# Optimization experiments

Measured on AMD Instinct MI355X. Metric: run time of the kernel, lower is better.

Reference implementation:

```python
import jax, jax.numpy as jnp
import numpy as np

B, S, D, H = 32, 2048, 512, 512

def setup_inputs() -> dict:
    key = jax.random.key(0)
    kx, kq, kk, kv = jax.random.split(key, 4)
    scale = 1.0 / np.sqrt(D)
    x = jax.random.normal(kx, (B, S, D), dtype=jnp.float32)
    Wq = jax.random.normal(kq, (D, H), dtype=jnp.float32) * scale
    Wk = jax.random.normal(kk, (D, H), dtype=jnp.float32) * scale
    Wv = jax.random.normal(kv, (D, H), dtype=jnp.float32) * scale
    return {"x": x, "Wq": Wq, "Wk": Wk, "Wv": Wv}

def reference(x, Wq, Wk, Wv):
    # Linear projections (bias=False)
    q = jnp.einsum('bsd,dh->bsh', x, Wq)
    k = jnp.einsum('bsd,dh->bsh', x, Wk)
    v = jnp.einsum('bsd,dh->bsh', x, Wv)
    # Pairwise KL(p_i || q_j) with p = softmax(q_i), q = softmax(k_j):
    #   KL = sum_h p_i log p_i  -  sum_h p_i log q_j
    # The first term is a per-row negative entropy; the second is a GEMM,
    # avoiding the original O(S^2) Python double loop.
    logp = jax.nn.log_softmax(q, axis=-1)          # [B,S,H]
    p = jnp.exp(logp)
    logq = jax.nn.log_softmax(k, axis=-1)          # [B,S,H]
    neg_ent = jnp.sum(p * logp, axis=-1)           # [B,S]
    cross = jnp.einsum('bih,bjh->bij', p, logq)    # [B,S,S]
    kl_divs = neg_ent[:, :, None] - cross          # [B,S,S]
    attn_weights = jax.nn.softmax(-kl_divs, axis=-1)
    attn_output = jnp.einsum('bij,bjh->bih', attn_weights, v)
    return attn_output
```

## Files before the change

kernel.cpp:

```cpp
#include <hip/hip_runtime.h>
#include <hip/hip_bf16.h>

typedef __bf16 bf16x8 __attribute__((ext_vector_type(8)));
typedef float  f32x4  __attribute__((ext_vector_type(4)));

#define NB 32
#define NS 2048
#define ND 512
#define NH 512
#define NROWS (NB*NS)
#define L2E 1.44269504f

__device__ __forceinline__ void gload16(const void* g, void* l) {
  __builtin_amdgcn_global_load_lds((const __attribute__((address_space(1))) void*)g,
                                   (__attribute__((address_space(3))) void*)l, 16, 0, 0);
}

__global__ void prep_w(const float* __restrict__ Wq, const float* __restrict__ Wk,
                       const float* __restrict__ Wv, __bf16* __restrict__ wT) {
  int i = blockIdx.x * blockDim.x + threadIdx.x;
  const int total = 3 * ND * NH;
  for (; i < total; i += gridDim.x * blockDim.x) {
    int m = i / (ND * NH);
    int rem = i - m * (ND * NH);
    int h = rem >> 9;
    int d = rem & 511;
    const float* W = (m == 0) ? Wq : ((m == 1) ? Wk : Wv);
    wT[i] = (__bf16)W[(size_t)d * NH + h];
  }
}

#define K1_XOFF 0
#define K1_WOFF 65536
#define K1_REDM 131072
#define K1_REDS 132096
#define K1_LDS  133120

__global__ __launch_bounds__(512, 2)
void proj_kernel(const float* __restrict__ x, const __bf16* __restrict__ wT,
                 __bf16* __restrict__ p_out, __bf16* __restrict__ k_out,
                 float* __restrict__ L_out, __bf16* __restrict__ vt_out)
{
  __shared__ __align__(16) char smem[K1_LDS];
  char* xb = smem + K1_XOFF;
  char* wb = smem + K1_WOFF;
  float* redm = (float*)(smem + K1_REDM);
  float* reds = (float*)(smem + K1_REDS);

  const int tid = threadIdx.x;
  const int lane = tid & 63, l15 = lane & 15, g = lane >> 4;
  const int w = tid >> 6, rt = w & 1, cs = w >> 1;
  const int r0 = blockIdx.x * 64;
  const int b = r0 >> 11, s0 = r0 & (NS - 1);

  {
    int row = tid >> 3, sc = tid & 7;
    const float* xr = x + (size_t)(r0 + row) * ND;
    #pragma unroll
    for (int u = 0; u < 8; ++u) {
      int s = u * 8 + sc;
      float4 v0 = *(const float4*)(xr + s * 8);
      float4 v1 = *(const float4*)(xr + s * 8 + 4);
      bf16x8 cv;
      cv[0]=(__bf16)v0.x; cv[1]=(__bf16)v0.y; cv[2]=(__bf16)v0.z; cv[3]=(__bf16)v0.w;
      cv[4]=(__bf16)v1.x; cv[5]=(__bf16)v1.y; cv[6]=(__bf16)v1.z; cv[7]=(__bf16)v1.w;
      *(bf16x8*)(xb + row * 1024 + ((s ^ (row & 7)) * 16)) = cv;
    }
  }
  {
    #pragma unroll
    for (int u = 0; u < 4; ++u) {
      int sid = u * 512 + tid, h = sid >> 2, gg = sid & 3;
      gload16(wT + (size_t)h * ND + ((gg ^ ((h >> 1) & 3)) * 8), wb + sid * 16);
    }
  }
  __syncthreads();

  for (int m = 0; m < 3; ++m) {
    f32x4 acc[2][8];
    #pragma unroll
    for (int i2 = 0; i2 < 2; ++i2)
      #pragma unroll
      for (int ht = 0; ht < 8; ++ht) acc[i2][ht] = (f32x4){0.f,0.f,0.f,0.f};

    for (int step = 0; step < 16; ++step) {
      int gs = m * 16 + step;
      char* wcur = wb + (gs & 1) * 32768;
      if (gs + 1 < 48) {
        int gn = gs + 1, mn = gn >> 4, sn = gn & 15;
        const __bf16* wsrc = wT + (size_t)mn * (ND * NH) + sn * 32;
        char* wdst = wb + (gn & 1) * 32768;
        #pragma unroll
        for (int u = 0; u < 4; ++u) {
          int sid = u * 512 + tid, h = sid >> 2, gg = sid & 3;
          gload16(wsrc + (size_t)h * ND + ((gg ^ ((h >> 1) & 3)) * 8), wdst + sid * 16);
        }
      }
      bf16x8 a0, a1;
      {
        int ar = rt * 32 + l15;
        a0 = *(const bf16x8*)(xb + ar * 1024 + (((step * 4 + g) ^ (ar & 7)) * 16));
        ar += 16;
        a1 = *(const bf16x8*)(xb + ar * 1024 + (((step * 4 + g) ^ (ar & 7)) * 16));
      }
      #pragma unroll
      for (int ht = 0; ht < 8; ++ht) {
        int h = cs * 128 + ht * 16 + l15;
        bf16x8 bb = *(const bf16x8*)(wcur + h * 64 + ((g ^ ((h >> 1) & 3)) * 16));
        acc[0][ht] = __builtin_amdgcn_mfma_f32_16x16x32_bf16(a0, bb, acc[0][ht], 0, 0, 0);
        acc[1][ht] = __builtin_amdgcn_mfma_f32_16x16x32_bf16(a1, bb, acc[1][ht], 0, 0, 0);
      }
      __syncthreads();
    }

    if (m == 2) {
      #pragma unroll
      for (int i2 = 0; i2 < 2; ++i2) {
        int sgg = (s0 >> 3) + rt * 4 + i2 * 2 + (g >> 1);
        size_t basep = ((size_t)(b * 256 + sgg)) * 512;
        #pragma unroll
        for (int ht = 0; ht < 8; ++ht) {
          int h = cs * 128 + ht * 16 + l15;
          union { __bf16 h4[4]; ushort4 u4; } cv;
          #pragma unroll
          for (int r = 0; r < 4; ++r) cv.h4[r] = (__bf16)acc[i2][ht][r];
          *(ushort4*)(vt_out + (basep + h) * 8 + (g & 1) * 4) = cv.u4;
        }
      }
    } else {
      float mrow[2][4], tsum[2][4];
      #pragma unroll
      for (int i2 = 0; i2 < 2; ++i2)
        #pragma unroll
        for (int r = 0; r < 4; ++r) {
          float v = acc[i2][0][r];
          #pragma unroll
          for (int ht = 1; ht < 8; ++ht) v = fmaxf(v, acc[i2][ht][r]);
          v = fmaxf(v, __shfl_xor(v, 1)); v = fmaxf(v, __shfl_xor(v, 2));
          v = fmaxf(v, __shfl_xor(v, 4)); v = fmaxf(v, __shfl_xor(v, 8));
          if (l15 == 0) redm[cs * 64 + rt * 32 + i2 * 16 + g * 4 + r] = v;
        }
      __syncthreads();
      #pragma unroll
      for (int i2 = 0; i2 < 2; ++i2)
        #pragma unroll
        for (int r = 0; r < 4; ++r) {
          int row = rt * 32 + i2 * 16 + g * 4 + r;
          mrow[i2][r] = fmaxf(fmaxf(redm[row], redm[64 + row]),
                              fmaxf(redm[128 + row], redm[192 + row]));
        }
      #pragma unroll
      for (int i2 = 0; i2 < 2; ++i2)
        #pragma unroll
        for (int r = 0; r < 4; ++r) {
          float s = 0.f;
          #pragma unroll
          for (int ht = 0; ht < 8; ++ht) s += exp2f((acc[i2][ht][r] - mrow[i2][r]) * L2E);
          s += __shfl_xor(s, 1); s += __shfl_xor(s, 2);
          s += __shfl_xor(s, 4); s += __shfl_xor(s, 8);
          if (l15 == 0) reds[cs * 64 + rt * 32 + i2 * 16 + g * 4 + r] = s;
        }
      __syncthreads();
      #pragma unroll
      for (int i2 = 0; i2 < 2; ++i2)
        #pragma unroll
        for (int r = 0; r < 4; ++r) {
          int row = rt * 32 + i2 * 16 + g * 4 + r;
          tsum[i2][r] = reds[row] + reds[64 + row] + reds[128 + row] + reds[192 + row];
        }
      __bf16* dst = (m == 0) ? p_out : k_out;
      if (m == 0) {
        #pragma unroll
        for (int i2 = 0; i2 < 2; ++i2) {
          float inv[4];
          #pragma unroll
          for (int r = 0; r < 4; ++r) inv[r] = 1.f / tsum[i2][r];
          #pragma unroll
          for (int ht = 0; ht < 8; ++ht) {
            int col = cs * 128 + ht * 16 + l15;
            #pragma unroll
            for (int r = 0; r < 4; ++r) {
              int row = rt * 32 + i2 * 16 + g * 4 + r;
              dst[(size_t)(r0 + row) * NH + col] =
                  (__bf16)(exp2f((acc[i2][ht][r] - mrow[i2][r]) * L2E) * inv[r]);
            }
          }
        }
      } else {
        #pragma unroll
        for (int i2 = 0; i2 < 2; ++i2)
          #pragma unroll
          for (int ht = 0; ht < 8; ++ht) {
            int col = cs * 128 + ht * 16 + l15;
            #pragma unroll
            for (int r = 0; r < 4; ++r) {
              int row = rt * 32 + i2 * 16 + g * 4 + r;
              dst[(size_t)(r0 + row) * NH + col] = (__bf16)acc[i2][ht][r];
            }
          }
        if (cs == 0 && l15 == 0) {
          #pragma unroll
          for (int i2 = 0; i2 < 2; ++i2)
            #pragma unroll
            for (int r = 0; r < 4; ++r) {
              int row = rt * 32 + i2 * 16 + g * 4 + r;
              L_out[r0 + row] = mrow[i2][r] + __logf(tsum[i2][r]);
            }
        }
      }
      __syncthreads();
    }
  }
}

#define QOFF 0
#define KOFF 65536
#define PSTR 512
#define LOFF 131072
#define LREDOFF 139264
#define A_LDS 140288

__global__ __launch_bounds__(512, 2)
void attn_kernel(const __bf16* __restrict__ p_all, const __bf16* __restrict__ k_all,
                 const float* __restrict__ L_all, const __bf16* __restrict__ vt_all,
                 float* __restrict__ out)
{
  __shared__ __align__(16) char smem[A_LDS];
  char* Qb = smem + QOFF;
  char* Pb = smem + KOFF;
  float* Lld = (float*)(smem + LOFF);
  float* lred = (float*)(smem + LREDOFF);

  const int bid = blockIdx.x;
  const int b = ((bid >> 8) << 3) + (bid & 7);
  const int ib = (bid >> 3) & 31;
  const int i0 = ib * 64;

  const __bf16* Pg = p_all + (size_t)b * NS * NH;
  const __bf16* Kg = k_all + (size_t)b * NS * NH;
  const float*  Lg = L_all + (size_t)b * NS;
  const __bf16* Vg = vt_all + (size_t)b * (256 * 512 * 8);
  float* Og = out + ((size_t)b * NS + i0) * NH;

  const int tid = threadIdx.x;
  const int lane = tid & 63, l15 = lane & 15, g = lane >> 4;
  const int w = tid >> 6;
  const int ig = w >> 2, jg = w & 3;
  const int hs = w * 64;
  const int xr = l15 & 7;

  *(float4*)(Lld + tid * 4) = *(const float4*)(Lg + tid * 4);
  #pragma unroll
  for (int u = 0; u < 8; ++u) {
    int sid = u * 512 + tid, row = sid >> 6, s = sid & 63;
    int sp = (s & 56) | ((s ^ row) & 7);
    gload16(Pg + (size_t)(i0 + row) * NH + sp * 8, Qb + sid * 16);
  }

  f32x4 o_[4][4];
  #pragma unroll
  for (int it = 0; it < 4; ++it)
    #pragma unroll
    for (int ht = 0; ht < 4; ++ht) o_[it][ht] = (f32x4){0.f,0.f,0.f,0.f};
  float lsum[2][4] = {{0.f,0.f,0.f,0.f},{0.f,0.f,0.f,0.f}};

  #define STAGEK(J0, KK, DST) { \
    _Pragma("unroll") \
    for (int u_ = 0; u_ < 4; ++u_) { \
      int sid_ = u_ * 512 + tid, jj_ = sid_ >> 3, ss_ = sid_ & 7; \
      gload16(Kg + (size_t)((J0) + jj_) * NH + (KK) * 64 + ((ss_ ^ (jj_ & 7)) * 8), \
              (DST) + sid_ * 16); \
    } }

  for (int outer = 0; outer < 8; ++outer) {
    const int j0 = outer * 256;
    __syncthreads();
    STAGEK(j0, 0, smem + KOFF);
    __syncthreads();

    f32x4 acc[2][4];
    #pragma unroll
    for (int it = 0; it < 2; ++it)
      #pragma unroll
      for (int jt = 0; jt < 4; ++jt) acc[it][jt] = (f32x4){0.f,0.f,0.f,0.f};

    for (int kk = 0; kk < 8; ++kk) {
      const char* rb = smem + KOFF + (kk & 1) * 32768;
      if (kk < 7) STAGEK(j0, kk + 1, smem + KOFF + ((kk + 1) & 1) * 32768);
      #pragma unroll
      for (int sub = 0; sub < 2; ++sub) {
        bf16x8 a0, a1, bf[4];
        {
          int row = ig * 32 + l15;
          int seg = kk * 8 + ((sub * 4 + g) ^ xr);
          a0 = *(const bf16x8*)(Qb + row * 1024 + seg * 16);
          a1 = *(const bf16x8*)(Qb + (row + 16) * 1024 + seg * 16);
        }
        #pragma unroll
        for (int jt = 0; jt < 4; ++jt) {
          int j = jg * 64 + jt * 16 + l15;
          bf[jt] = *(const bf16x8*)(rb + j * 128 + (((sub * 4 + g) ^ xr) * 16));
        }
        #pragma unroll
        for (int jt = 0; jt < 4; ++jt) {
          acc[0][jt] = __builtin_amdgcn_mfma_f32_16x16x32_bf16(a0, bf[jt], acc[0][jt], 0, 0, 0);
          acc[1][jt] = __builtin_amdgcn_mfma_f32_16x16x32_bf16(a1, bf[jt], acc[1][jt], 0, 0, 0);
        }
      }
      __syncthreads();
    }

    #pragma unroll
    for (int it = 0; it < 2; ++it) {
      #pragma unroll
      for (int jt = 0; jt < 4; ++jt) {
        float LB = Lld[j0 + jg * 64 + jt * 16 + l15] * L2E;
        #pragma unroll
        for (int r = 0; r < 4; ++r) {
          float pv = exp2f(acc[it][jt][r] * L2E - LB);
          lsum[it][r] += pv;
          float other = __shfl_xor(pv, 1);
          if ((l15 & 1) == 0) {
            union { __bf16 h; unsigned short u; } lo, hi;
            lo.h = (__bf16)pv; hi.h = (__bf16)other;
            unsigned int pk = (unsigned int)lo.u | ((unsigned int)hi.u << 16);
            int row = ig * 32 + it * 16 + g * 4 + r;
            int d = jg * 32 + jt * 8 + (l15 >> 1);
            int s2 = (d >> 2) ^ (row & 7);
            *(unsigned int*)(Pb + row * PSTR + s2 * 16 + (d & 3) * 4) = pk;
          }
        }
      }
    }
    __syncthreads();

    #define LOADV(DST, JKS) { \
      _Pragma("unroll") \
      for (int ht_ = 0; ht_ < 4; ++ht_) { \
        int h_ = hs + ht_ * 16 + l15; \
        int sg_ = outer * 32 + (JKS) * 4 + g; \
        (DST)[ht_] = *(const bf16x8*)(Vg + ((size_t)sg_ * 512 + h_) * 8); \
      } }
    #define PVSTEP(JKS, VF) { \
      _Pragma("unroll") \
      for (int it_ = 0; it_ < 4; ++it_) { \
        int row_ = it_ * 16 + l15; \
        int sp_ = ((JKS) * 4 + g) ^ xr; \
        bf16x8 pa_ = *(const bf16x8*)(Pb + row_ * PSTR + sp_ * 16); \
        _Pragma("unroll") \
        for (int ht_ = 0; ht_ < 4; ++ht_) \
          o_[it_][ht_] = __builtin_amdgcn_mfma_f32_16x16x32_bf16(pa_, (VF)[ht_], o_[it_][ht_], 0, 0, 0); \
      } }

    {
      bf16x8 vA[4], vB[4];
      LOADV(vA, 0);
      #pragma unroll
      for (int jks = 0; jks < 8; jks += 2) {
        LOADV(vB, jks + 1);
        PVSTEP(jks, vA);
        if (jks + 2 < 8) LOADV(vA, jks + 2);
        PVSTEP(jks + 1, vB);
      }
    }
  }

  #pragma unroll
  for (int it = 0; it < 2; ++it)
    #pragma unroll
    for (int r = 0; r < 4; ++r) {
      float v = lsum[it][r];
      v += __shfl_xor(v, 1); v += __shfl_xor(v, 2);
      v += __shfl_xor(v, 4); v += __shfl_xor(v, 8);
      if (l15 == 0) lred[jg * 64 + ig * 32 + it * 16 + g * 4 + r] = v;
    }
  __syncthreads();

  #pragma unroll
  for (int it = 0; it < 4; ++it) {
    float inv[4];
    #pragma unroll
    for (int r = 0; r < 4; ++r) {
      int row = it * 16 + g * 4 + r;
      inv[r] = 1.f / (lred[row] + lred[64 + row] + lred[128 + row] + lred[192 + row]);
    }
    #pragma unroll
    for (int ht = 0; ht < 4; ++ht)
      #pragma unroll
      for (int r = 0; r < 4; ++r) {
        int row = it * 16 + g * 4 + r;
        Og[(size_t)row * NH + hs + ht * 16 + l15] = o_[it][ht][r] * inv[r];
      }
  }
}

extern "C" void kernel_launch(void* const* d_in, const int* in_sizes, int n_in,
                              void* d_out, int out_size, void* d_ws, size_t ws_size,
                              hipStream_t stream) {
  const float* x  = (const float*)d_in[0];
  const float* Wq = (const float*)d_in[1];
  const float* Wk = (const float*)d_in[2];
  const float* Wv = (const float*)d_in[3];
  float* out = (float*)d_out;
  char* ws = (char*)d_ws;

  size_t off = 0;
  __bf16* wT   = (__bf16*)(ws + off); off += (size_t)3 * ND * NH * 2;
  __bf16* p_ws = (__bf16*)(ws + off); off += (size_t)NROWS * NH * 2;
  __bf16* k_ws = (__bf16*)(ws + off); off += (size_t)NROWS * NH * 2;
  __bf16* vt_ws= (__bf16*)(ws + off); off += (size_t)NROWS * NH * 2;
  float*  L_ws = (float*)(ws + off);  off += (size_t)NROWS * 4;

  prep_w<<<dim3(512), dim3(256), 0, stream>>>(Wq, Wk, Wv, wT);
  proj_kernel<<<dim3(1024), dim3(512), 0, stream>>>(x, wT, p_ws, k_ws, L_ws, vt_ws);
  attn_kernel<<<dim3(1024), dim3(512), 0, stream>>>(p_ws, k_ws, L_ws, vt_ws, out);
}
```

Baseline: 760.4 us.

## Pipeline K staging across outer tiles and re-tile projection warps

In the attention kernel, P gets its own LDS region instead of aliasing the K buffer. This lets the next outer tile's first K slice be prefetched during the PV phase, removing the per-outer barrier-and-load bubble. The L values are now read directly from global memory instead of being staged in LDS, and V fragments are triple-buffered in registers. The projection kernel changes its warp tiling from 2x4 (32 rows x 128 cols) to 1x8 (64 rows x 64 cols per warp), which alters register use and LDS read traffic. The cost is more LDS per block (163840 bytes for attention), which may limit occupancy.

```diff
diff --git a/kernel.cpp b/kernel.cpp
--- a/kernel.cpp
+++ b/kernel.cpp
@@ -33,8 +33,8 @@
 #define K1_XOFF 0
 #define K1_WOFF 65536
 #define K1_REDM 131072
-#define K1_REDS 132096
-#define K1_LDS  133120
+#define K1_REDS 133120
+#define K1_LDS  135168
 
 __global__ __launch_bounds__(512, 2)
 void proj_kernel(const float* __restrict__ x, const __bf16* __restrict__ wT,
@@ -49,7 +49,7 @@
 
   const int tid = threadIdx.x;
   const int lane = tid & 63, l15 = lane & 15, g = lane >> 4;
-  const int w = tid >> 6, rt = w & 1, cs = w >> 1;
+  const int cs = tid >> 6;
   const int r0 = blockIdx.x * 64;
   const int b = r0 >> 11, s0 = r0 & (NS - 1);
 
@@ -67,144 +67,143 @@
       *(bf16x8*)(xb + row * 1024 + ((s ^ (row & 7)) * 16)) = cv;
     }
   }
-  {
-    #pragma unroll
-    for (int u = 0; u < 4; ++u) {
-      int sid = u * 512 + tid, h = sid >> 2, gg = sid & 3;
-      gload16(wT + (size_t)h * ND + ((gg ^ ((h >> 1) & 3)) * 8), wb + sid * 16);
-    }
-  }
+  #define STAGEW(GS) { \
+    int mn_ = (GS) >> 4, sn_ = (GS) & 15; \
+    const __bf16* ws_ = wT + (size_t)mn_ * (ND * NH) + sn_ * 32; \
+    char* wd_ = wb + ((GS) & 1) * 32768; \
+    _Pragma("unroll") \
+    for (int u_ = 0; u_ < 4; ++u_) { \
+      int sid_ = u_ * 512 + tid, h_ = sid_ >> 2, gg_ = sid_ & 3; \
+      gload16(ws_ + (size_t)h_ * ND + ((gg_ ^ ((h_ >> 1) & 3)) * 8), wd_ + sid_ * 16); \
+    } }
+  STAGEW(0);
   __syncthreads();
 
   for (int m = 0; m < 3; ++m) {
-    f32x4 acc[2][8];
-    #pragma unroll
-    for (int i2 = 0; i2 < 2; ++i2)
-      #pragma unroll
-      for (int ht = 0; ht < 8; ++ht) acc[i2][ht] = (f32x4){0.f,0.f,0.f,0.f};
+    f32x4 acc[4][4];
+    #pragma unroll
+    for (int it = 0; it < 4; ++it)
+      #pragma unroll
+      for (int ht = 0; ht < 4; ++ht) acc[it][ht] = (f32x4){0.f,0.f,0.f,0.f};
 
     for (int step = 0; step < 16; ++step) {
       int gs = m * 16 + step;
-      char* wcur = wb + (gs & 1) * 32768;
-      if (gs + 1 < 48) {
-        int gn = gs + 1, mn = gn >> 4, sn = gn & 15;
-        const __bf16* wsrc = wT + (size_t)mn * (ND * NH) + sn * 32;
-        char* wdst = wb + (gn & 1) * 32768;
-        #pragma unroll
-        for (int u = 0; u < 4; ++u) {
-          int sid = u * 512 + tid, h = sid >> 2, gg = sid & 3;
-          gload16(wsrc + (size_t)h * ND + ((gg ^ ((h >> 1) & 3)) * 8), wdst + sid * 16);
-        }
-      }
-      bf16x8 a0, a1;
-      {
-        int ar = rt * 32 + l15;
-        a0 = *(const bf16x8*)(xb + ar * 1024 + (((step * 4 + g) ^ (ar & 7)) * 16));
-        ar += 16;
-        a1 = *(const bf16x8*)(xb + ar * 1024 + (((step * 4 + g) ^ (ar & 7)) * 16));
-      }
-      #pragma unroll
-      for (int ht = 0; ht < 8; ++ht) {
-        int h = cs * 128 + ht * 16 + l15;
-        bf16x8 bb = *(const bf16x8*)(wcur + h * 64 + ((g ^ ((h >> 1) & 3)) * 16));
-        acc[0][ht] = __builtin_amdgcn_mfma_f32_16x16x32_bf16(a0, bb, acc[0][ht], 0, 0, 0);
-        acc[1][ht] = __builtin_amdgcn_mfma_f32_16x16x32_bf16(a1, bb, acc[1][ht], 0, 0, 0);
-      }
+      const char* wcur = wb + (gs & 1) * 32768;
+      if (gs + 1 < 48) STAGEW(gs + 1);
+      bf16x8 a[4], bq[4];
+      #pragma unroll
+      for (int it = 0; it < 4; ++it) {
+        int row = it * 16 + l15;
+        a[it] = *(const bf16x8*)(xb + row * 1024 + (((step * 4 + g) ^ (row & 7)) * 16));
+      }
+      #pragma unroll
+      for (int ht = 0; ht < 4; ++ht) {
+        int h = cs * 64 + ht * 16 + l15;
+        bq[ht] = *(const bf16x8*)(wcur + h * 64 + ((g ^ ((h >> 1) & 3)) * 16));
+      }
+      #pragma unroll
+      for (int it = 0; it < 4; ++it)
+        #pragma unroll
+        for (int ht = 0; ht < 4; ++ht)
+          acc[it][ht] = __builtin_amdgcn_mfma_f32_16x16x32_bf16(a[it], bq[ht], acc[it][ht], 0, 0, 0);
       __syncthreads();
     }
 
     if (m == 2) {
       #pragma unroll
-      for (int i2 = 0; i2 < 2; ++i2) {
-        int sgg = (s0 >> 3) + rt * 4 + i2 * 2 + (g >> 1);
+      for (int it = 0; it < 4; ++it) {
+        int sgg = (s0 >> 3) + it * 2 + (g >> 1);
         size_t basep = ((size_t)(b * 256 + sgg)) * 512;
         #pragma unroll
-        for (int ht = 0; ht < 8; ++ht) {
-          int h = cs * 128 + ht * 16 + l15;
+        for (int ht = 0; ht < 4; ++ht) {
+          int h = cs * 64 + ht * 16 + l15;
           union { __bf16 h4[4]; ushort4 u4; } cv;
           #pragma unroll
-          for (int r = 0; r < 4; ++r) cv.h4[r] = (__bf16)acc[i2][ht][r];
+          for (int r = 0; r < 4; ++r) cv.h4[r] = (__bf16)acc[it][ht][r];
           *(ushort4*)(vt_out + (basep + h) * 8 + (g & 1) * 4) = cv.u4;
         }
       }
     } else {
-      float mrow[2][4], tsum[2][4];
-      #pragma unroll
-      for (int i2 = 0; i2 < 2; ++i2)
+      #pragma unroll
+      for (int it = 0; it < 4; ++it)
         #pragma unroll
         for (int r = 0; r < 4; ++r) {
-          float v = acc[i2][0][r];
-          #pragma unroll
-          for (int ht = 1; ht < 8; ++ht) v = fmaxf(v, acc[i2][ht][r]);
+          float v = acc[it][0][r];
+          #pragma unroll
+          for (int ht = 1; ht < 4; ++ht) v = fmaxf(v, acc[it][ht][r]);
           v = fmaxf(v, __shfl_xor(v, 1)); v = fmaxf(v, __shfl_xor(v, 2));
           v = fmaxf(v, __shfl_xor(v, 4)); v = fmaxf(v, __shfl_xor(v, 8));
-          if (l15 == 0) redm[cs * 64 + rt * 32 + i2 * 16 + g * 4 + r] = v;
+          if (l15 == 0) redm[cs * 64 + it * 16 + g * 4 + r] = v;
         }
       __syncthreads();
-      #pragma unroll
-      for (int i2 = 0; i2 < 2; ++i2)
+      float mrow[4][4];
+      #pragma unroll
+      for (int it = 0; it < 4; ++it)
         #pragma unroll
         for (int r = 0; r < 4; ++r) {
-          int row = rt * 32 + i2 * 16 + g * 4 + r;
-          mrow[i2][r] = fmaxf(fmaxf(redm[row], redm[64 + row]),
-                              fmaxf(redm[128 + row], redm[192 + row]));
-        }
-      #pragma unroll
-      for (int i2 = 0; i2 < 2; ++i2)
+          int row = it * 16 + g * 4 + r;
+          float mv = redm[row];
+          #pragma unroll
+          for (int w2 = 1; w2 < 8; ++w2) mv = fmaxf(mv, redm[w2 * 64 + row]);
+          mrow[it][r] = mv;
+        }
+      #pragma unroll
+      for (int it = 0; it < 4; ++it)
         #pragma unroll
         for (int r = 0; r < 4; ++r) {
           float s = 0.f;
           #pragma unroll
-          for (int ht = 0; ht < 8; ++ht) s += exp2f((acc[i2][ht][r] - mrow[i2][r]) * L2E);
+          for (int ht = 0; ht < 4; ++ht) s += exp2f((acc[it][ht][r] - mrow[it][r]) * L2E);
           s += __shfl_xor(s, 1); s += __shfl_xor(s, 2);
           s += __shfl_xor(s, 4); s += __shfl_xor(s, 8);
-          if (l15 == 0) reds[cs * 64 + rt * 32 + i2 * 16 + g * 4 + r] = s;
+          if (l15 == 0) reds[cs * 64 + it * 16 + g * 4 + r] = s;
         }
       __syncthreads();
-      #pragma unroll
-      for (int i2 = 0; i2 < 2; ++i2)
+      float tsum[4][4];
+      #pragma unroll
+      for (int it = 0; it < 4; ++it)
         #pragma unroll
         for (int r = 0; r < 4; ++r) {
-          int row = rt * 32 + i2 * 16 + g * 4 + r;
-          tsum[i2][r] = reds[row] + reds[64 + row] + reds[128 + row] + reds[192 + row];
+          int row = it * 16 + g * 4 + r;
+          float s = reds[row];
+          #pragma unroll
+          for (int w2 = 1; w2 < 8; ++w2) s += reds[w2 * 64 + row];
+          tsum[it][r] = s;
         }
       __bf16* dst = (m == 0) ? p_out : k_out;
       if (m == 0) {
         #pragma unroll
-        for (int i2 = 0; i2 < 2; ++i2) {
-          float inv[4];
-          #pragma unroll
-          for (int r = 0; r < 4; ++r) inv[r] = 1.f / tsum[i2][r];
-          #pragma unroll
-          for (int ht = 0; ht < 8; ++ht) {
-            int col = cs * 128 + ht * 16 + l15;
+        for (int it = 0; it < 4; ++it)
+          #pragma unroll
+          for (int r = 0; r < 4; ++r) {
+            int row = it * 16 + g * 4 + r;
+            float inv = 1.f / tsum[it][r];
+            #pragma unroll
+            for (int ht = 0; ht < 4; ++ht) {
+              int col = cs * 64 + ht * 16 + l15;
+              dst[(size_t)(r0 + row) * NH + col] =
+                  (__bf16)(exp2f((acc[it][ht][r] - mrow[it][r]) * L2E) * inv);
+            }
+          }
+      } else {
+        #pragma unroll
+        for (int it = 0; it < 4; ++it)
+          #pragma unroll
+          for (int ht = 0; ht < 4; ++ht) {
+            int col = cs * 64 + ht * 16 + l15;
             #pragma unroll
             for (int r = 0; r < 4; ++r) {
-              int row = rt * 32 + i2 * 16 + g * 4 + r;
-              dst[(size_t)(r0 + row) * NH + col] =
-                  (__bf16)(exp2f((acc[i2][ht][r] - mrow[i2][r]) * L2E) * inv[r]);
-            }
-          }
-        }
-      } else {
-        #pragma unroll
-        for (int i2 = 0; i2 < 2; ++i2)
-          #pragma unroll
-          for (int ht = 0; ht < 8; ++ht) {
-            int col = cs * 128 + ht * 16 + l15;
-            #pragma unroll
-            for (int r = 0; r < 4; ++r) {
-              int row = rt * 32 + i2 * 16 + g * 4 + r;
-              dst[(size_t)(r0 + row) * NH + col] = (__bf16)acc[i2][ht][r];
+              int row = it * 16 + g * 4 + r;
+              dst[(size_t)(r0 + row) * NH + col] = (__bf16)acc[it][ht][r];
             }
           }
         if (cs == 0 && l15 == 0) {
           #pragma unroll
-          for (int i2 = 0; i2 < 2; ++i2)
+          for (int it = 0; it < 4; ++it)
             #pragma unroll
             for (int r = 0; r < 4; ++r) {
-              int row = rt * 32 + i2 * 16 + g * 4 + r;
-              L_out[r0 + row] = mrow[i2][r] + __logf(tsum[i2][r]);
+              int row = it * 16 + g * 4 + r;
+              L_out[r0 + row] = mrow[it][r] + __logf(tsum[it][r]);
             }
         }
       }
@@ -215,10 +214,9 @@
 
 #define QOFF 0
 #define KOFF 65536
+#define POFF 131072
 #define PSTR 512
-#define LOFF 131072
-#define LREDOFF 139264
-#define A_LDS 140288
+#define A_LDS 163840
 
 __global__ __launch_bounds__(512, 2)
 void attn_kernel(const __bf16* __restrict__ p_all, const __bf16* __restrict__ k_all,
@@ -227,9 +225,8 @@
 {
   __shared__ __align__(16) char smem[A_LDS];
   char* Qb = smem + QOFF;
-  char* Pb = smem + KOFF;
-  float* Lld = (float*)(smem + LOFF);
-  float* lred = (float*)(smem + LREDOFF);
+  char* Pb = smem + POFF;
+  float* lred = (float*)(smem + POFF);
 
   const int bid = blockIdx.x;
   const int b = ((bid >> 8) << 3) + (bid & 7);
@@ -249,13 +246,24 @@
   const int hs = w * 64;
   const int xr = l15 & 7;
 
-  *(float4*)(Lld + tid * 4) = *(const float4*)(Lg + tid * 4);
+  #define STAGE(SS) { \
+    int j0_ = ((SS) >> 3) * 256, kh_ = (SS) & 7; \
+    char* kd_ = smem + KOFF + ((SS) & 1) * 32768; \
+    _Pragma("unroll") \
+    for (int u_ = 0; u_ < 4; ++u_) { \
+      int sid_ = u_ * 512 + tid, jj_ = sid_ >> 3, s8_ = sid_ & 7; \
+      gload16(Kg + (size_t)(j0_ + jj_) * NH + kh_ * 64 + ((s8_ ^ (jj_ & 7)) * 8), \
+              kd_ + sid_ * 16); \
+    } }
+
   #pragma unroll
   for (int u = 0; u < 8; ++u) {
     int sid = u * 512 + tid, row = sid >> 6, s = sid & 63;
     int sp = (s & 56) | ((s ^ row) & 7);
     gload16(Pg + (size_t)(i0 + row) * NH + sp * 8, Qb + sid * 16);
   }
+  STAGE(0);
+  __syncthreads();
 
   f32x4 o_[4][4];
   #pragma unroll
@@ -264,115 +272,111 @@
     for (int ht = 0; ht < 4; ++ht) o_[it][ht] = (f32x4){0.f,0.f,0.f,0.f};
   float lsum[2][4] = {{0.f,0.f,0.f,0.f},{0.f,0.f,0.f,0.f}};
 
-  #define STAGEK(J0, KK, DST) { \
+  #define LOADV(DST, JKS) { \
     _Pragma("unroll") \
-    for (int u_ = 0; u_ < 4; ++u_) { \
-      int sid_ = u_ * 512 + tid, jj_ = sid_ >> 3, ss_ = sid_ & 7; \
-      gload16(Kg + (size_t)((J0) + jj_) * NH + (KK) * 64 + ((ss_ ^ (jj_ & 7)) * 8), \
-              (DST) + sid_ * 16); \
+    for (int ht_ = 0; ht_ < 4; ++ht_) { \
+      int h_ = hs + ht_ * 16 + l15; \
+      int sg_ = outer * 32 + (JKS) * 4 + g; \
+      (DST)[ht_] = *(const bf16x8*)(Vg + ((size_t)sg_ * 512 + h_) * 8); \
+    } }
+  #define PVSTEP(JKS, VF) { \
+    _Pragma("unroll") \
+    for (int it_ = 0; it_ < 4; ++it_) { \
+      int row_ = it_ * 16 + l15; \
+      int sp_ = ((JKS) * 4 + g) ^ xr; \
+      bf16x8 pa_ = *(const bf16x8*)(Pb + row_ * PSTR + sp_ * 16); \
+      _Pragma("unroll") \
+      for (int ht_ = 0; ht_ < 4; ++ht_) \
+        o_[it_][ht_] = __builtin_amdgcn_mfma_f32_16x16x32_bf16(pa_, (VF)[ht_], o_[it_][ht_], 0, 0, 0); \
     } }
 
   for (int outer = 0; outer < 8; ++outer) {
     const int j0 = outer * 256;
-    __syncthreads();
-    STAGEK(j0, 0, smem + KOFF);
-    __syncthreads();
-
     f32x4 acc[2][4];
     #pragma unroll
-    for (int it = 0; it < 2; ++it)
-      #pragma unroll
-      for (int jt = 0; jt < 4; ++jt) acc[it][jt] = (f32x4){0.f,0.f,0.f,0.f};
-
+    for (int i2 = 0; i2 < 2; ++i2)
+      #pragma unroll
+      for (int jt = 0; jt < 4; ++jt) acc[i2][jt] = (f32x4){0.f,0.f,0.f,0.f};
+
+    #pragma unroll
     for (int kk = 0; kk < 8; ++kk) {
-      const char* rb = smem + KOFF + (kk & 1) * 32768;
-      if (kk < 7) STAGEK(j0, kk + 1, smem + KOFF + ((kk + 1) & 1) * 32768);
-      #pragma unroll
-      for (int sub = 0; sub < 2; ++sub) {
-        bf16x8 a0, a1, bf[4];
-        {
-          int row = ig * 32 + l15;
-          int seg = kk * 8 + ((sub * 4 + g) ^ xr);
-          a0 = *(const bf16x8*)(Qb + row * 1024 + seg * 16);
-          a1 = *(const bf16x8*)(Qb + (row + 16) * 1024 + seg * 16);
-        }
+      const int ss = outer * 8 + kk;
+      if (!(kk == 0 && outer > 0) && ss < 63) STAGE(ss + 1);
+      const char* rb = smem + KOFF + (ss & 1) * 32768;
+      bf16x8 aq[2][2], bq[2][4];
+      #pragma unroll
+      for (int i2 = 0; i2 < 2; ++i2) {
+        int row = ig * 32 + i2 * 16 + l15;
+        #pragma unroll
+        for (int sub = 0; sub < 2; ++sub)
+          aq[i2][sub] = *(const bf16x8*)(Qb + row * 1024 +
+                         (((kk * 8 + sub * 4 + g) ^ (row & 7)) * 16));
+      }
+      #pragma unroll
+      for (int sub = 0; sub < 2; ++sub)
         #pragma unroll
         for (int jt = 0; jt < 4; ++jt) {
           int j = jg * 64 + jt * 16 + l15;
-          bf[jt] = *(const bf16x8*)(rb + j * 128 + (((sub * 4 + g) ^ xr) * 16));
-        }
-        #pragma unroll
-        for (int jt = 0; jt < 4; ++jt) {
-          acc[0][jt] = __builtin_amdgcn_mfma_f32_16x16x32_bf16(a0, bf[jt], acc[0][jt], 0, 0, 0);
-          acc[1][jt] = __builtin_amdgcn_mfma_f32_16x16x32_bf16(a1, bf[jt], acc[1][jt], 0, 0, 0);
-        }
-      }
+          bq[sub][jt] = *(const bf16x8*)(rb + j * 128 + (((sub * 4 + g) ^ xr) * 16));
+        }
+      #pragma unroll
+      for (int sub = 0; sub < 2; ++sub)
+        #pragma unroll
+        for (int i2 = 0; i2 < 2; ++i2)
+          #pragma unroll
+          for (int jt = 0; jt < 4; ++jt)
+            acc[i2][jt] = __builtin_amdgcn_mfma_f32_16x16x32_bf16(aq[i2][sub], bq[sub][jt], acc[i2][jt], 0, 0, 0);
       __syncthreads();
     }
 
-    #pragma unroll
-    for (int it = 0; it < 2; ++it) {
-      #pragma unroll
-      for (int jt = 0; jt < 4; ++jt) {
-        float LB = Lld[j0 + jg * 64 + jt * 16 + l15] * L2E;
-        #pragma unroll
-        for (int r = 0; r < 4; ++r) {
-          float pv = exp2f(acc[it][jt][r] * L2E - LB);
-          lsum[it][r] += pv;
-          float other = __shfl_xor(pv, 1);
-          if ((l15 & 1) == 0) {
-            union { __bf16 h; unsigned short u; } lo, hi;
-            lo.h = (__bf16)pv; hi.h = (__bf16)other;
-            unsigned int pk = (unsigned int)lo.u | ((unsigned int)hi.u << 16);
-            int row = ig * 32 + it * 16 + g * 4 + r;
-            int d = jg * 32 + jt * 8 + (l15 >> 1);
-            int s2 = (d >> 2) ^ (row & 7);
-            *(unsigned int*)(Pb + row * PSTR + s2 * 16 + (d & 3) * 4) = pk;
+    {
+      float LB[4];
+      #pragma unroll
+      for (int jt = 0; jt < 4; ++jt) LB[jt] = Lg[j0 + jg * 64 + jt * 16 + l15] * L2E;
+      #pragma unroll
+      for (int i2 = 0; i2 < 2; ++i2)
+        #pragma unroll
+        for (int jt = 0; jt < 4; ++jt)
+          #pragma unroll
+          for (int r = 0; r < 4; ++r) {
+            float pv = exp2f(acc[i2][jt][r] * L2E - LB[jt]);
+            lsum[i2][r] += pv;
+            float other = __shfl_xor(pv, 1);
+            if ((l15 & 1) == 0) {
+              union { __bf16 h; unsigned short u; } lo, hi;
+              lo.h = (__bf16)pv; hi.h = (__bf16)other;
+              unsigned int pk = (unsigned int)lo.u | ((unsigned int)hi.u << 16);
+              int row = ig * 32 + i2 * 16 + g * 4 + r;
+              int d = jg * 32 + jt * 8 + (l15 >> 1);
+              int s2 = (d >> 2) ^ (row & 7);
+              *(unsigned int*)(Pb + row * PSTR + s2 * 16 + (d & 3) * 4) = pk;
+            }
           }
-        }
-      }
-    }
+    }
+    bf16x8 vA[4], vB[4], vC[4];
+    LOADV(vA, 0); LOADV(vB, 1); LOADV(vC, 2);
     __syncthreads();
-
-    #define LOADV(DST, JKS) { \
-      _Pragma("unroll") \
-      for (int ht_ = 0; ht_ < 4; ++ht_) { \
-        int h_ = hs + ht_ * 16 + l15; \
-        int sg_ = outer * 32 + (JKS) * 4 + g; \
-        (DST)[ht_] = *(const bf16x8*)(Vg + ((size_t)sg_ * 512 + h_) * 8); \
-      } }
-    #define PVSTEP(JKS, VF) { \
-      _Pragma("unroll") \
-      for (int it_ = 0; it_ < 4; ++it_) { \
-        int row_ = it_ * 16 + l15; \
-        int sp_ = ((JKS) * 4 + g) ^ xr; \
-        bf16x8 pa_ = *(const bf16x8*)(Pb + row_ * PSTR + sp_ * 16); \
-        _Pragma("unroll") \
-        for (int ht_ = 0; ht_ < 4; ++ht_) \
-          o_[it_][ht_] = __builtin_amdgcn_mfma_f32_16x16x32_bf16(pa_, (VF)[ht_], o_[it_][ht_], 0, 0, 0); \
-      } }
-
-    {
-      bf16x8 vA[4], vB[4];
-      LOADV(vA, 0);
-      #pragma unroll
-      for (int jks = 0; jks < 8; jks += 2) {
-        LOADV(vB, jks + 1);
-        PVSTEP(jks, vA);
-        if (jks + 2 < 8) LOADV(vA, jks + 2);
-        PVSTEP(jks + 1, vB);
-      }
-    }
-  }
-
+    if (outer < 7) STAGE(outer * 8 + 9);
+
+    PVSTEP(0, vA); LOADV(vA, 3);
+    PVSTEP(1, vB); LOADV(vB, 4);
+    PVSTEP(2, vC); LOADV(vC, 5);
+    PVSTEP(3, vA); LOADV(vA, 6);
+    PVSTEP(4, vB); LOADV(vB, 7);
+    PVSTEP(5, vC);
+    PVSTEP(6, vA);
+    PVSTEP(7, vB);
+  }
+
+  __syncthreads();
   #pragma unroll
-  for (int it = 0; it < 2; ++it)
+  for (int i2 = 0; i2 < 2; ++i2)
     #pragma unroll
     for (int r = 0; r < 4; ++r) {
-      float v = lsum[it][r];
+      float v = lsum[i2][r];
       v += __shfl_xor(v, 1); v += __shfl_xor(v, 2);
       v += __shfl_xor(v, 4); v += __shfl_xor(v, 8);
-      if (l15 == 0) lred[jg * 64 + ig * 32 + it * 16 + g * 4 + r] = v;
+      if (l15 == 0) lred[jg * 64 + ig * 32 + i2 * 16 + g * 4 + r] = v;
     }
   __syncthreads();
 
```

Measured after the change: 849.6 us. 1.12x slower.

## Triple-buffer K tiles across outer iterations and overlap staging with softmax and PV

Applied to the files above, without the earlier changes.

Replaces the per-outer-iteration K double buffer with a three-slot ring that keeps two stages in flight across outer-loop boundaries. The P tile now reuses the just-consumed K slot instead of having its own region. The L values are read directly from global memory instead of a preloaded LDS copy. Full __syncthreads are replaced with explicit waitcnt plus s_barrier, and MFMA sections are wrapped in s_setprio. This is meant to hide K load latency and remove pipeline restart bubbles, at the cost of more LDS, tighter hand-managed synchronization and a risk of subtle buffer-reuse hazards.

```diff
diff --git a/kernel.cpp b/kernel.cpp
--- a/kernel.cpp
+++ b/kernel.cpp
@@ -216,9 +216,7 @@
 #define QOFF 0
 #define KOFF 65536
 #define PSTR 512
-#define LOFF 131072
-#define LREDOFF 139264
-#define A_LDS 140288
+#define A_LDS 163840
 
 __global__ __launch_bounds__(512, 2)
 void attn_kernel(const __bf16* __restrict__ p_all, const __bf16* __restrict__ k_all,
@@ -227,9 +225,7 @@
 {
   __shared__ __align__(16) char smem[A_LDS];
   char* Qb = smem + QOFF;
-  char* Pb = smem + KOFF;
-  float* Lld = (float*)(smem + LOFF);
-  float* lred = (float*)(smem + LREDOFF);
+  float* lred = (float*)(smem + KOFF);
 
   const int bid = blockIdx.x;
   const int b = ((bid >> 8) << 3) + (bid & 7);
@@ -249,13 +245,24 @@
   const int hs = w * 64;
   const int xr = l15 & 7;
 
-  *(float4*)(Lld + tid * 4) = *(const float4*)(Lg + tid * 4);
+  #define STAGE(SS) { \
+    int j0_ = ((SS) >> 3) * 256, kh_ = (SS) & 7; \
+    char* kd_ = smem + KOFF + ((SS) % 3) * 32768; \
+    _Pragma("unroll") \
+    for (int u_ = 0; u_ < 4; ++u_) { \
+      int sid_ = u_ * 512 + tid, jj_ = sid_ >> 3, s8_ = sid_ & 7; \
+      gload16(Kg + (size_t)(j0_ + jj_) * NH + kh_ * 64 + ((s8_ ^ (jj_ & 7)) * 8), \
+              kd_ + sid_ * 16); \
+    } }
+
   #pragma unroll
   for (int u = 0; u < 8; ++u) {
     int sid = u * 512 + tid, row = sid >> 6, s = sid & 63;
     int sp = (s & 56) | ((s ^ row) & 7);
     gload16(Pg + (size_t)(i0 + row) * NH + sp * 8, Qb + sid * 16);
   }
+  STAGE(0);
+  STAGE(1);
 
   f32x4 o_[4][4];
   #pragma unroll
@@ -264,115 +271,122 @@
     for (int ht = 0; ht < 4; ++ht) o_[it][ht] = (f32x4){0.f,0.f,0.f,0.f};
   float lsum[2][4] = {{0.f,0.f,0.f,0.f},{0.f,0.f,0.f,0.f}};
 
-  #define STAGEK(J0, KK, DST) { \
+  #define LOADV(DST, JKS) { \
     _Pragma("unroll") \
-    for (int u_ = 0; u_ < 4; ++u_) { \
-      int sid_ = u_ * 512 + tid, jj_ = sid_ >> 3, ss_ = sid_ & 7; \
-      gload16(Kg + (size_t)((J0) + jj_) * NH + (KK) * 64 + ((ss_ ^ (jj_ & 7)) * 8), \
-              (DST) + sid_ * 16); \
+    for (int ht_ = 0; ht_ < 4; ++ht_) { \
+      int h_ = hs + ht_ * 16 + l15; \
+      int sg_ = outer * 32 + (JKS) * 4 + g; \
+      (DST)[ht_] = *(const bf16x8*)(Vg + ((size_t)sg_ * 512 + h_) * 8); \
     } }
+  #define PVSTEP(JKS, VF) { \
+    __builtin_amdgcn_s_setprio(1); \
+    _Pragma("unroll") \
+    for (int it_ = 0; it_ < 4; ++it_) { \
+      int row_ = it_ * 16 + l15; \
+      int sp_ = ((JKS) * 4 + g) ^ xr; \
+      bf16x8 pa_ = *(const bf16x8*)(Pb + row_ * PSTR + sp_ * 16); \
+      _Pragma("unroll") \
+      for (int ht_ = 0; ht_ < 4; ++ht_) \
+        o_[it_][ht_] = __builtin_amdgcn_mfma_f32_16x16x32_bf16(pa_, (VF)[ht_], o_[it_][ht_], 0, 0, 0); \
+    } \
+    __builtin_amdgcn_s_setprio(0); }
 
   for (int outer = 0; outer < 8; ++outer) {
     const int j0 = outer * 256;
-    __syncthreads();
-    STAGEK(j0, 0, smem + KOFF);
-    __syncthreads();
-
     f32x4 acc[2][4];
     #pragma unroll
-    for (int it = 0; it < 2; ++it)
-      #pragma unroll
-      for (int jt = 0; jt < 4; ++jt) acc[it][jt] = (f32x4){0.f,0.f,0.f,0.f};
-
+    for (int i2 = 0; i2 < 2; ++i2)
+      #pragma unroll
+      for (int jt = 0; jt < 4; ++jt) acc[i2][jt] = (f32x4){0.f,0.f,0.f,0.f};
+
+    #pragma unroll
     for (int kk = 0; kk < 8; ++kk) {
-      const char* rb = smem + KOFF + (kk & 1) * 32768;
-      if (kk < 7) STAGEK(j0, kk + 1, smem + KOFF + ((kk + 1) & 1) * 32768);
+      const int ss = outer * 8 + kk;
+      asm volatile("s_waitcnt vmcnt(4)" ::: "memory");
+      __builtin_amdgcn_sched_barrier(0);
+      __builtin_amdgcn_s_barrier();
+      __builtin_amdgcn_sched_barrier(0);
+      if (ss + 2 < 64) STAGE(ss + 2);
+      const char* rb = smem + KOFF + (ss % 3) * 32768;
       #pragma unroll
       for (int sub = 0; sub < 2; ++sub) {
-        bf16x8 a0, a1, bf[4];
+        bf16x8 a0, a1, bq[4];
         {
-          int row = ig * 32 + l15;
-          int seg = kk * 8 + ((sub * 4 + g) ^ xr);
-          a0 = *(const bf16x8*)(Qb + row * 1024 + seg * 16);
-          a1 = *(const bf16x8*)(Qb + (row + 16) * 1024 + seg * 16);
+          int row0 = ig * 32 + l15;
+          int seg = kk * 8 + sub * 4 + g;
+          a0 = *(const bf16x8*)(Qb + row0 * 1024 + ((seg ^ (row0 & 7)) * 16));
+          a1 = *(const bf16x8*)(Qb + (row0 + 16) * 1024 + ((seg ^ ((row0 + 16) & 7)) * 16));
         }
         #pragma unroll
         for (int jt = 0; jt < 4; ++jt) {
           int j = jg * 64 + jt * 16 + l15;
-          bf[jt] = *(const bf16x8*)(rb + j * 128 + (((sub * 4 + g) ^ xr) * 16));
-        }
+          bq[jt] = *(const bf16x8*)(rb + j * 128 + (((sub * 4 + g) ^ xr) * 16));
+        }
+        __builtin_amdgcn_s_setprio(1);
         #pragma unroll
         for (int jt = 0; jt < 4; ++jt) {
-          acc[0][jt] = __builtin_amdgcn_mfma_f32_16x16x32_bf16(a0, bf[jt], acc[0][jt], 0, 0, 0);
-          acc[1][jt] = __builtin_amdgcn_mfma_f32_16x16x32_bf16(a1, bf[jt], acc[1][jt], 0, 0, 0);
-        }
-      }
-      __syncthreads();
-    }
-
-    #pragma unroll
-    for (int it = 0; it < 2; ++it) {
-      #pragma unroll
-      for (int jt = 0; jt < 4; ++jt) {
-        float LB = Lld[j0 + jg * 64 + jt * 16 + l15] * L2E;
-        #pragma unroll
-        for (int r = 0; r < 4; ++r) {
-          float pv = exp2f(acc[it][jt][r] * L2E - LB);
-          lsum[it][r] += pv;
-          float other = __shfl_xor(pv, 1);
-          if ((l15 & 1) == 0) {
-            union { __bf16 h; unsigned short u; } lo, hi;
-            lo.h = (__bf16)pv; hi.h = (__bf16)other;
-            unsigned int pk = (unsigned int)lo.u | ((unsigned int)hi.u << 16);
-            int row = ig * 32 + it * 16 + g * 4 + r;
-            int d = jg * 32 + jt * 8 + (l15 >> 1);
-            int s2 = (d >> 2) ^ (row & 7);
-            *(unsigned int*)(Pb + row * PSTR + s2 * 16 + (d & 3) * 4) = pk;
+          acc[0][jt] = __builtin_amdgcn_mfma_f32_16x16x32_bf16(a0, bq[jt], acc[0][jt], 0, 0, 0);
+          acc[1][jt] = __builtin_amdgcn_mfma_f32_16x16x32_bf16(a1, bq[jt], acc[1][jt], 0, 0, 0);
+        }
+        __builtin_amdgcn_s_setprio(0);
+      }
+    }
+
+    __builtin_amdgcn_sched_barrier(0);
+    __builtin_amdgcn_s_barrier();
+    __builtin_amdgcn_sched_barrier(0);
+    char* Pb = smem + KOFF + ((outer * 8 + 7) % 3) * 32768;
+
+    {
+      float LB[4];
+      #pragma unroll
+      for (int jt = 0; jt < 4; ++jt) LB[jt] = Lg[j0 + jg * 64 + jt * 16 + l15] * L2E;
+      #pragma unroll
+      for (int i2 = 0; i2 < 2; ++i2)
+        #pragma unroll
+        for (int jt = 0; jt < 4; ++jt)
+          #pragma unroll
+          for (int r = 0; r < 4; ++r) {
+            float pv = exp2f(acc[i2][jt][r] * L2E - LB[jt]);
+            lsum[i2][r] += pv;
+            float other = __shfl_xor(pv, 1);
+            if ((l15 & 1) == 0) {
+              union { __bf16 h; unsigned short u; } lo, hi;
+              lo.h = (__bf16)pv; hi.h = (__bf16)other;
+              unsigned int pk = (unsigned int)lo.u | ((unsigned int)hi.u << 16);
+              int row = ig * 32 + i2 * 16 + g * 4 + r;
+              int d = jg * 32 + jt * 8 + (l15 >> 1);
+              int s2 = (d >> 2) ^ (row & 7);
+              *(unsigned int*)(Pb + row * PSTR + s2 * 16 + (d & 3) * 4) = pk;
+            }
           }
-        }
-      }
-    }
-    __syncthreads();
-
-    #define LOADV(DST, JKS) { \
-      _Pragma("unroll") \
-      for (int ht_ = 0; ht_ < 4; ++ht_) { \
-        int h_ = hs + ht_ * 16 + l15; \
-        int sg_ = outer * 32 + (JKS) * 4 + g; \
-        (DST)[ht_] = *(const bf16x8*)(Vg + ((size_t)sg_ * 512 + h_) * 8); \
-      } }
-    #define PVSTEP(JKS, VF) { \
-      _Pragma("unroll") \
-      for (int it_ = 0; it_ < 4; ++it_) { \
-        int row_ = it_ * 16 + l15; \
-        int sp_ = ((JKS) * 4 + g) ^ xr; \
-        bf16x8 pa_ = *(const bf16x8*)(Pb + row_ * PSTR + sp_ * 16); \
-        _Pragma("unroll") \
-        for (int ht_ = 0; ht_ < 4; ++ht_) \
-          o_[it_][ht_] = __builtin_amdgcn_mfma_f32_16x16x32_bf16(pa_, (VF)[ht_], o_[it_][ht_], 0, 0, 0); \
-      } }
-
-    {
-      bf16x8 vA[4], vB[4];
-      LOADV(vA, 0);
-      #pragma unroll
-      for (int jks = 0; jks < 8; jks += 2) {
-        LOADV(vB, jks + 1);
-        PVSTEP(jks, vA);
-        if (jks + 2 < 8) LOADV(vA, jks + 2);
-        PVSTEP(jks + 1, vB);
-      }
-    }
-  }
-
+    }
+    bf16x8 vA[4], vB[4];
+    LOADV(vA, 0); LOADV(vB, 1);
+    asm volatile("s_waitcnt lgkmcnt(0)" ::: "memory");
+    __builtin_amdgcn_sched_barrier(0);
+    __builtin_amdgcn_s_barrier();
+    __builtin_amdgcn_sched_barrier(0);
+
+    PVSTEP(0, vA); LOADV(vA, 2);
+    PVSTEP(1, vB); LOADV(vB, 3);
+    PVSTEP(2, vA); LOADV(vA, 4);
+    PVSTEP(3, vB); LOADV(vB, 5);
+    PVSTEP(4, vA); LOADV(vA, 6);
+    PVSTEP(5, vB); LOADV(vB, 7);
+    PVSTEP(6, vA);
+    PVSTEP(7, vB);
+  }
+
+  __syncthreads();
   #pragma unroll
-  for (int it = 0; it < 2; ++it)
+  for (int i2 = 0; i2 < 2; ++i2)
     #pragma unroll
     for (int r = 0; r < 4; ++r) {
-      float v = lsum[it][r];
+      float v = lsum[i2][r];
       v += __shfl_xor(v, 1); v += __shfl_xor(v, 2);
       v += __shfl_xor(v, 4); v += __shfl_xor(v, 8);
-      if (l15 == 0) lred[jg * 64 + ig * 32 + it * 16 + g * 4 + r] = v;
+      if (l15 == 0) lred[jg * 64 + ig * 32 + i2 * 16 + g * 4 + r] = v;
     }
   __syncthreads();
 
```

Measured after the change: 660.4 us. -13.1%, faster.
